# Performance work log

Measured on AMD Instinct MI355X. Metric: run time of the kernel, lower is better.

The kernel has to match this reference:

```python
import jax, jax.numpy as jnp
import numpy as np


def setup_inputs() -> dict:
    key = jax.random.key(0)
    k1, k2 = jax.random.split(key)
    B, N, D = 4, 2048, 1024
    context = jax.random.normal(k1, (B, N, D), dtype=jnp.float32)
    # Dense(embedding_dim*3): kernel [D, 3D], bias [3D] (glorot-ish scale)
    W_qkv = jax.random.normal(k2, (D, 3 * D), dtype=jnp.float32) * (1.0 / np.sqrt(D))
    b_qkv = jnp.zeros((3 * D,), dtype=jnp.float32)
    return {"context": context, "W_qkv": W_qkv, "b_qkv": b_qkv}


def reference(context, W_qkv, b_qkv):
    B, N, D = context.shape
    qkv = context @ W_qkv + b_qkv                       # [B, N, 3D]
    q, k, v = jnp.split(qkv, 3, axis=-1)                # each [B, N, D]
    scores = jnp.einsum("bnd,bmd->bnm", q, k)           # [B, N, N]
    # Faithful quirk: original divides by sqrt(scores.shape[-1]) == sqrt(N)
    scores = scores / jnp.asarray(np.sqrt(N), dtype=scores.dtype)
    causal = jnp.tril(jnp.ones((N, N), dtype=jnp.float32))  # lower-triangular
    scores = jnp.where(causal == 0, -jnp.inf, scores)
    probs = jax.nn.softmax(scores, axis=-1)             # [B, N, N]
    out = jnp.einsum("bnm,bmd->bnd", probs, v)          # [B, N, D]
    return out
```

## Files before the change

kernel.cpp:

```cpp
#include <hip/hip_runtime.h>
#include <cstdint>
#include <cstddef>


typedef __attribute__((ext_vector_type(8))) __bf16 bf16x8;
typedef __attribute__((ext_vector_type(4))) float f32x4;

__device__ inline unsigned short f2bf(float f) {
  unsigned u = __float_as_uint(f);
  u = (u + 0x7FFFu + ((u >> 16) & 1u)) >> 16;
  return (unsigned short)u;
}

__device__ inline void gld16(const void* g, void* l) {
  __builtin_amdgcn_global_load_lds(
      (const __attribute__((address_space(1))) unsigned int*)g,
      (__attribute__((address_space(3))) unsigned int*)l, 16, 0, 0);
}

__device__ inline void mma_mainloop(const unsigned short* Abase, long strideA,
                                    const unsigned short* Bbase, long strideB,
                                    int kIters, f32x4 acc[4][4]) {
  __shared__ unsigned short As[128 * 64];
  __shared__ unsigned short Bs[128 * 64];
  const int tid = threadIdx.x;
  const int lane = tid & 63;
  const int wave = tid >> 6;
  const int ry = (wave >> 1) * 64;
  const int rx = (wave & 1) * 64;
  const int lrow = lane >> 3;
  const int lchunk = (lane & 7) ^ lrow;
  const int lcol = lchunk * 8;

#pragma unroll
  for (int mi = 0; mi < 4; mi++)
#pragma unroll
    for (int nj = 0; nj < 4; nj++) acc[mi][nj] = (f32x4)(0.f);

  for (int kt = 0; kt < kIters; kt++) {
    const int k0 = kt * 64;
    __syncthreads();
#pragma unroll
    for (int c = 0; c < 4; c++) {
      const int q = wave * 4 + c;
      const int row = q * 8 + lrow;
      gld16(Abase + (size_t)row * strideA + k0 + lcol, &As[q * 512]);
      gld16(Bbase + (size_t)row * strideB + k0 + lcol, &Bs[q * 512]);
    }
    __syncthreads();
#pragma unroll
    for (int kk = 0; kk < 64; kk += 32) {
      const int cbase = (kk >> 3) + (lane >> 4);
      const int csw = ((cbase ^ (lane & 7)) << 3);
      bf16x8 a[4], b[4];
#pragma unroll
      for (int mi = 0; mi < 4; mi++)
        a[mi] = *(const bf16x8*)&As[(ry + mi * 16 + (lane & 15)) * 64 + csw];
#pragma unroll
      for (int nj = 0; nj < 4; nj++)
        b[nj] = *(const bf16x8*)&Bs[(rx + nj * 16 + (lane & 15)) * 64 + csw];
#pragma unroll
      for (int mi = 0; mi < 4; mi++)
#pragma unroll
        for (int nj = 0; nj < 4; nj++)
          acc[mi][nj] = __builtin_amdgcn_mfma_f32_16x16x32_bf16(a[mi], b[nj], acc[mi][nj], 0, 0, 0);
    }
  }
}


__global__ void k_convert(const float* __restrict__ x, unsigned short* __restrict__ y, int n4) {
  int i = blockIdx.x * blockDim.x + threadIdx.x;
  if (i >= n4) return;
  float4 v = ((const float4*)x)[i];
  ushort4 o;
  o.x = f2bf(v.x); o.y = f2bf(v.y); o.z = f2bf(v.z); o.w = f2bf(v.w);
  ((ushort4*)y)[i] = o;
}

__global__ void k_transpose_w(const float* __restrict__ W, unsigned short* __restrict__ Wt) {
  __shared__ unsigned short sm[64 * 65];
  const int n0 = blockIdx.x * 64;
  const int k0 = blockIdx.y * 64;
  for (int i = threadIdx.x; i < 4096; i += 256) {
    int r = i >> 6, c = i & 63;
    sm[c * 65 + r] = f2bf(W[(size_t)(k0 + r) * 3072 + n0 + c]);
  }
  __syncthreads();
  for (int i = threadIdx.x; i < 4096; i += 256) {
    int r = i >> 6, c = i & 63;
    Wt[(size_t)(n0 + r) * 1024 + k0 + c] = sm[r * 65 + c];
  }
}

__global__ void k_transpose_v(const unsigned short* __restrict__ qkv, unsigned short* __restrict__ vT) {
  __shared__ unsigned short sm[64 * 65];
  const int b = blockIdx.z;
  const int d0 = blockIdx.x * 64;
  const int n0 = blockIdx.y * 64;
  const unsigned short* src = qkv + ((size_t)b * 2048) * 3072 + 2048;
  for (int i = threadIdx.x; i < 4096; i += 256) {
    int r = i >> 6, c = i & 63;
    sm[c * 65 + r] = src[(size_t)(n0 + r) * 3072 + d0 + c];
  }
  __syncthreads();
  unsigned short* dst = vT + ((size_t)b * 1024) * 2048;
  for (int i = threadIdx.x; i < 4096; i += 256) {
    int r = i >> 6, c = i & 63;
    dst[(size_t)(d0 + r) * 2048 + n0 + c] = sm[r * 65 + c];
  }
}


__global__ __launch_bounds__(256) void k_gemm_qkv(const unsigned short* __restrict__ A,
                                                  const unsigned short* __restrict__ Bt,
                                                  const float* __restrict__ bias,
                                                  unsigned short* __restrict__ C) {
  f32x4 acc[4][4];
  const int tN0 = blockIdx.x * 128;
  const int tM0 = blockIdx.y * 128;
  mma_mainloop(A + (size_t)tM0 * 1024, 1024, Bt + (size_t)tN0 * 1024, 1024, 16, acc);
  const int lane = threadIdx.x & 63, wave = threadIdx.x >> 6;
  const int ry = (wave >> 1) * 64, rx = (wave & 1) * 64;
  const int col0 = lane & 15, rq = lane >> 4;
#pragma unroll
  for (int mi = 0; mi < 4; mi++)
#pragma unroll
    for (int nj = 0; nj < 4; nj++) {
      const int n = tN0 + rx + nj * 16 + col0;
      const float bv = bias[n];
#pragma unroll
      for (int r = 0; r < 4; r++) {
        const int m = tM0 + ry + mi * 16 + rq * 4 + r;
        C[(size_t)m * 3072 + n] = f2bf(acc[mi][nj][r] + bv);
      }
    }
}

__global__ __launch_bounds__(256) void k_scores(const unsigned short* __restrict__ qkv,
                                                unsigned short* __restrict__ P,
                                                float* __restrict__ l, float scale) {
  const int t = blockIdx.x, b = blockIdx.z;
  int qb = (int)((sqrtf(8.0f * (float)t + 1.0f) - 1.0f) * 0.5f);
  while (qb * (qb + 1) / 2 > t) qb--;
  while ((qb + 1) * (qb + 2) / 2 <= t) qb++;
  const int kb = t - qb * (qb + 1) / 2;
  f32x4 acc[4][4];
  const unsigned short* A = qkv + ((size_t)(b * 2048 + qb * 128)) * 3072;
  const unsigned short* B = qkv + ((size_t)(b * 2048 + kb * 128)) * 3072 + 1024;
  mma_mainloop(A, 3072, B, 3072, 16, acc);
  const int lane = threadIdx.x & 63, wave = threadIdx.x >> 6;
  const int ry = (wave >> 1) * 64, rx = (wave & 1) * 64;
  const int col0 = lane & 15, rq = lane >> 4;
  unsigned short* Pb = P + ((size_t)(b * 2048 + qb * 128)) * 2048 + (size_t)kb * 128;
  float* lb = l + b * 2048 + qb * 128;
#pragma unroll
  for (int mi = 0; mi < 4; mi++) {
#pragma unroll
    for (int r = 0; r < 4; r++) {
      const int m_local = ry + mi * 16 + rq * 4 + r;
      const int qi = qb * 128 + m_local;
      float rowpart = 0.f;
#pragma unroll
      for (int nj = 0; nj < 4; nj++) {
        const int n_local = rx + nj * 16 + col0;
        const int kj = kb * 128 + n_local;
        float p = 0.f;
        if (kj <= qi) p = __expf(acc[mi][nj][r] * scale);
        rowpart += p;
        Pb[(size_t)m_local * 2048 + n_local] = f2bf(p);
      }
      for (int off = 1; off < 16; off <<= 1) rowpart += __shfl_xor(rowpart, off, 64);
      if (col0 == 0) atomicAdd(&lb[m_local], rowpart);
    }
  }
}

__global__ __launch_bounds__(256) void k_pv(const unsigned short* __restrict__ P,
                                            const unsigned short* __restrict__ vT,
                                            const float* __restrict__ l,
                                            float* __restrict__ out) {
  const int db = blockIdx.x, qb = blockIdx.y, b = blockIdx.z;
  f32x4 acc[4][4];
  const unsigned short* A = P + ((size_t)(b * 2048 + qb * 128)) * 2048;
  const unsigned short* B = vT + ((size_t)(b * 1024 + db * 128)) * 2048;
  mma_mainloop(A, 2048, B, 2048, (qb + 1) * 2, acc);
  const int lane = threadIdx.x & 63, wave = threadIdx.x >> 6;
  const int ry = (wave >> 1) * 64, rx = (wave & 1) * 64;
  const int col0 = lane & 15, rq = lane >> 4;
  const float* lb = l + b * 2048 + qb * 128;
  float* ob = out + ((size_t)(b * 2048 + qb * 128)) * 1024 + db * 128;
#pragma unroll
  for (int mi = 0; mi < 4; mi++)
#pragma unroll
    for (int r = 0; r < 4; r++) {
      const int m_local = ry + mi * 16 + rq * 4 + r;
      const float inv = 1.0f / lb[m_local];
#pragma unroll
      for (int nj = 0; nj < 4; nj++) {
        const int n_local = rx + nj * 16 + col0;
        ob[(size_t)m_local * 1024 + n_local] = acc[mi][nj][r] * inv;
      }
    }
}


extern "C" void kernel_launch(void* const* d_in, const int* in_sizes, int n_in,
                              void* d_out, int out_size, void* d_ws, size_t ws_size,
                              hipStream_t stream) {
  const float* ctx  = (const float*)d_in[0];
  const float* W    = (const float*)d_in[1];
  const float* bias = (const float*)d_in[2];
  float* out = (float*)d_out;

  char* ws = (char*)d_ws;
  unsigned short* Actx = (unsigned short*)(ws + 0);
  unsigned short* Wt   = (unsigned short*)(ws + 16777216);
  unsigned short* qkv  = (unsigned short*)(ws + 23068672);
  unsigned short* vT   = (unsigned short*)(ws + 73400320);
  unsigned short* P    = (unsigned short*)(ws + 90177536);
  float*          lsum = (float*)(ws + 123731968);

  hipMemsetAsync(lsum, 0, 4 * 2048 * sizeof(float), stream);
  k_convert<<<8192, 256, 0, stream>>>(ctx, Actx, (8192 * 1024) / 4);
  k_transpose_w<<<dim3(48, 16), 256, 0, stream>>>(W, Wt);
  k_gemm_qkv<<<dim3(24, 64), 256, 0, stream>>>(Actx, Wt, bias, qkv);
  k_transpose_v<<<dim3(16, 32, 4), 256, 0, stream>>>(qkv, vT);
  k_scores<<<dim3(136, 1, 4), 256, 0, stream>>>(qkv, P, lsum, 0.022097086912079608f);
  k_pv<<<dim3(8, 16, 4), 256, 0, stream>>>(P, vT, lsum, out);
}
```

Measured before the change: 262.3 us.

## Fuse V transpose into QKV GEMM epilogue and vectorize epilogue stores

The QKV projection now writes Q and K to a packed buffer and writes V already transposed through its epilogue, which removes the separate V-transpose kernel and its extra global traffic. A templated MFMA operand swap makes each lane's four accumulators contiguous along the output column. Epilogues in all three GEMMs can then use 4-wide vector stores, and the row-sum shuffle reduction shrinks. The PV kernel also reverses the query-block order for half the batches to balance the causal workload across the grid.

New measurement: 257.0 us. 1.02x faster.

```diff
diff --git a/kernel.cpp b/kernel.cpp
--- a/kernel.cpp
+++ b/kernel.cpp
@@ -18,19 +18,18 @@
       (__attribute__((address_space(3))) unsigned int*)l, 16, 0, 0);
 }
 
-__device__ inline void mma_mainloop(const unsigned short* Abase, long strideA,
+template <bool SWAP>
+__device__ inline void mma_mainloop(unsigned short* As, unsigned short* Bs,
+                                    const unsigned short* Abase, long strideA,
                                     const unsigned short* Bbase, long strideB,
                                     int kIters, f32x4 acc[4][4]) {
-  __shared__ unsigned short As[128 * 64];
-  __shared__ unsigned short Bs[128 * 64];
   const int tid = threadIdx.x;
   const int lane = tid & 63;
   const int wave = tid >> 6;
   const int ry = (wave >> 1) * 64;
   const int rx = (wave & 1) * 64;
   const int lrow = lane >> 3;
-  const int lchunk = (lane & 7) ^ lrow;
-  const int lcol = lchunk * 8;
+  const int lcol = ((lane & 7) ^ lrow) * 8;
 
 #pragma unroll
   for (int mi = 0; mi < 4; mi++)
@@ -63,7 +62,9 @@
       for (int mi = 0; mi < 4; mi++)
 #pragma unroll
         for (int nj = 0; nj < 4; nj++)
-          acc[mi][nj] = __builtin_amdgcn_mfma_f32_16x16x32_bf16(a[mi], b[nj], acc[mi][nj], 0, 0, 0);
+          acc[mi][nj] = SWAP
+            ? __builtin_amdgcn_mfma_f32_16x16x32_bf16(b[nj], a[mi], acc[mi][nj], 0, 0, 0)
+            : __builtin_amdgcn_mfma_f32_16x16x32_bf16(a[mi], b[nj], acc[mi][nj], 0, 0, 0);
     }
   }
 }
@@ -93,86 +94,103 @@
   }
 }
 
-__global__ void k_transpose_v(const unsigned short* __restrict__ qkv, unsigned short* __restrict__ vT) {
-  __shared__ unsigned short sm[64 * 65];
-  const int b = blockIdx.z;
-  const int d0 = blockIdx.x * 64;
-  const int n0 = blockIdx.y * 64;
-  const unsigned short* src = qkv + ((size_t)b * 2048) * 3072 + 2048;
-  for (int i = threadIdx.x; i < 4096; i += 256) {
-    int r = i >> 6, c = i & 63;
-    sm[c * 65 + r] = src[(size_t)(n0 + r) * 3072 + d0 + c];
-  }
-  __syncthreads();
-  unsigned short* dst = vT + ((size_t)b * 1024) * 2048;
-  for (int i = threadIdx.x; i < 4096; i += 256) {
-    int r = i >> 6, c = i & 63;
-    dst[(size_t)(d0 + r) * 2048 + n0 + c] = sm[r * 65 + c];
-  }
-}
-
 
 __global__ __launch_bounds__(256) void k_gemm_qkv(const unsigned short* __restrict__ A,
-                                                  const unsigned short* __restrict__ Bt,
+                                                  const unsigned short* __restrict__ Wt,
                                                   const float* __restrict__ bias,
-                                                  unsigned short* __restrict__ C) {
+                                                  unsigned short* __restrict__ qk,
+                                                  unsigned short* __restrict__ vT) {
+  __shared__ unsigned short As[128 * 64];
+  __shared__ unsigned short Bs[128 * 64];
   f32x4 acc[4][4];
-  const int tN0 = blockIdx.x * 128;
   const int tM0 = blockIdx.y * 128;
-  mma_mainloop(A + (size_t)tM0 * 1024, 1024, Bt + (size_t)tN0 * 1024, 1024, 16, acc);
   const int lane = threadIdx.x & 63, wave = threadIdx.x >> 6;
   const int ry = (wave >> 1) * 64, rx = (wave & 1) * 64;
-  const int col0 = lane & 15, rq = lane >> 4;
-#pragma unroll
-  for (int mi = 0; mi < 4; mi++)
+  const int l16 = lane & 15, rq = lane >> 4;
+
+  if (blockIdx.x < 16) {
+    const int tN0 = blockIdx.x * 128;
+    mma_mainloop<true>(As, Bs, A + (size_t)tM0 * 1024, 1024,
+                       Wt + (size_t)tN0 * 1024, 1024, 16, acc);
+#pragma unroll
+    for (int mi = 0; mi < 4; mi++) {
+      const int m = tM0 + ry + mi * 16 + l16;
+#pragma unroll
+      for (int nj = 0; nj < 4; nj++) {
+        const int n = tN0 + rx + nj * 16 + rq * 4;
+        const float4 bv = *(const float4*)&bias[n];
+        ushort4 o;
+        o.x = f2bf(acc[mi][nj][0] + bv.x);
+        o.y = f2bf(acc[mi][nj][1] + bv.y);
+        o.z = f2bf(acc[mi][nj][2] + bv.z);
+        o.w = f2bf(acc[mi][nj][3] + bv.w);
+        *(ushort4*)&qk[(size_t)m * 2048 + n] = o;
+      }
+    }
+  } else {
+    const int tN0 = (blockIdx.x - 16) * 128;
+    mma_mainloop<false>(As, Bs, A + (size_t)tM0 * 1024, 1024,
+                        Wt + (size_t)(2048 + tN0) * 1024, 1024, 16, acc);
 #pragma unroll
     for (int nj = 0; nj < 4; nj++) {
-      const int n = tN0 + rx + nj * 16 + col0;
-      const float bv = bias[n];
-#pragma unroll
-      for (int r = 0; r < 4; r++) {
-        const int m = tM0 + ry + mi * 16 + rq * 4 + r;
-        C[(size_t)m * 3072 + n] = f2bf(acc[mi][nj][r] + bv);
+      const int d = tN0 + rx + nj * 16 + l16;
+      const float bv = bias[2048 + d];
+#pragma unroll
+      for (int mi = 0; mi < 4; mi++) {
+        const int m = tM0 + ry + mi * 16 + rq * 4;
+        const int b = m >> 11, ns = m & 2047;
+        ushort4 o;
+        o.x = f2bf(acc[mi][nj][0] + bv);
+        o.y = f2bf(acc[mi][nj][1] + bv);
+        o.z = f2bf(acc[mi][nj][2] + bv);
+        o.w = f2bf(acc[mi][nj][3] + bv);
+        *(ushort4*)&vT[((size_t)(b * 1024 + d)) * 2048 + ns] = o;
       }
     }
-}
-
-__global__ __launch_bounds__(256) void k_scores(const unsigned short* __restrict__ qkv,
+  }
+}
+
+__global__ __launch_bounds__(256) void k_scores(const unsigned short* __restrict__ qk,
                                                 unsigned short* __restrict__ P,
                                                 float* __restrict__ l, float scale) {
+  __shared__ unsigned short As[128 * 64];
+  __shared__ unsigned short Bs[128 * 64];
   const int t = blockIdx.x, b = blockIdx.z;
   int qb = (int)((sqrtf(8.0f * (float)t + 1.0f) - 1.0f) * 0.5f);
   while (qb * (qb + 1) / 2 > t) qb--;
   while ((qb + 1) * (qb + 2) / 2 <= t) qb++;
   const int kb = t - qb * (qb + 1) / 2;
   f32x4 acc[4][4];
-  const unsigned short* A = qkv + ((size_t)(b * 2048 + qb * 128)) * 3072;
-  const unsigned short* B = qkv + ((size_t)(b * 2048 + kb * 128)) * 3072 + 1024;
-  mma_mainloop(A, 3072, B, 3072, 16, acc);
+  const unsigned short* Aq = qk + ((size_t)(b * 2048 + qb * 128)) * 2048;
+  const unsigned short* Bk = qk + ((size_t)(b * 2048 + kb * 128)) * 2048 + 1024;
+  mma_mainloop<true>(As, Bs, Aq, 2048, Bk, 2048, 16, acc);
   const int lane = threadIdx.x & 63, wave = threadIdx.x >> 6;
   const int ry = (wave >> 1) * 64, rx = (wave & 1) * 64;
-  const int col0 = lane & 15, rq = lane >> 4;
+  const int l16 = lane & 15, rq = lane >> 4;
   unsigned short* Pb = P + ((size_t)(b * 2048 + qb * 128)) * 2048 + (size_t)kb * 128;
   float* lb = l + b * 2048 + qb * 128;
 #pragma unroll
   for (int mi = 0; mi < 4; mi++) {
-#pragma unroll
-    for (int r = 0; r < 4; r++) {
-      const int m_local = ry + mi * 16 + rq * 4 + r;
-      const int qi = qb * 128 + m_local;
-      float rowpart = 0.f;
-#pragma unroll
-      for (int nj = 0; nj < 4; nj++) {
-        const int n_local = rx + nj * 16 + col0;
-        const int kj = kb * 128 + n_local;
-        float p = 0.f;
-        if (kj <= qi) p = __expf(acc[mi][nj][r] * scale);
+    const int m_local = ry + mi * 16 + l16;
+    const int qi = qb * 128 + m_local;
+    float rowpart = 0.f;
+#pragma unroll
+    for (int nj = 0; nj < 4; nj++) {
+      const int n_base = rx + nj * 16 + rq * 4;
+      ushort4 o;
+      float p;
+#pragma unroll
+      for (int r = 0; r < 4; r++) {
+        const int kj = kb * 128 + n_base + r;
+        p = (kj <= qi) ? __expf(acc[mi][nj][r] * scale) : 0.f;
         rowpart += p;
-        Pb[(size_t)m_local * 2048 + n_local] = f2bf(p);
+        ((unsigned short*)&o)[r] = f2bf(p);
       }
-      for (int off = 1; off < 16; off <<= 1) rowpart += __shfl_xor(rowpart, off, 64);
-      if (col0 == 0) atomicAdd(&lb[m_local], rowpart);
-    }
+      *(ushort4*)&Pb[(size_t)m_local * 2048 + n_base] = o;
+    }
+    rowpart += __shfl_xor(rowpart, 16, 64);
+    rowpart += __shfl_xor(rowpart, 32, 64);
+    if (rq == 0) atomicAdd(&lb[m_local], rowpart);
   }
 }
 
@@ -180,28 +198,35 @@
                                             const unsigned short* __restrict__ vT,
                                             const float* __restrict__ l,
                                             float* __restrict__ out) {
-  const int db = blockIdx.x, qb = blockIdx.y, b = blockIdx.z;
+  __shared__ unsigned short As[128 * 64];
+  __shared__ unsigned short Bs[128 * 64];
+  const int db = blockIdx.x, b = blockIdx.z;
+  int qb = blockIdx.y;
+  if (b & 2) qb = 15 - qb;
   f32x4 acc[4][4];
-  const unsigned short* A = P + ((size_t)(b * 2048 + qb * 128)) * 2048;
-  const unsigned short* B = vT + ((size_t)(b * 1024 + db * 128)) * 2048;
-  mma_mainloop(A, 2048, B, 2048, (qb + 1) * 2, acc);
+  const unsigned short* Ap = P + ((size_t)(b * 2048 + qb * 128)) * 2048;
+  const unsigned short* Bv = vT + ((size_t)(b * 1024 + db * 128)) * 2048;
+  mma_mainloop<true>(As, Bs, Ap, 2048, Bv, 2048, (qb + 1) * 2, acc);
   const int lane = threadIdx.x & 63, wave = threadIdx.x >> 6;
   const int ry = (wave >> 1) * 64, rx = (wave & 1) * 64;
-  const int col0 = lane & 15, rq = lane >> 4;
+  const int l16 = lane & 15, rq = lane >> 4;
   const float* lb = l + b * 2048 + qb * 128;
   float* ob = out + ((size_t)(b * 2048 + qb * 128)) * 1024 + db * 128;
 #pragma unroll
-  for (int mi = 0; mi < 4; mi++)
-#pragma unroll
-    for (int r = 0; r < 4; r++) {
-      const int m_local = ry + mi * 16 + rq * 4 + r;
-      const float inv = 1.0f / lb[m_local];
-#pragma unroll
-      for (int nj = 0; nj < 4; nj++) {
-        const int n_local = rx + nj * 16 + col0;
-        ob[(size_t)m_local * 1024 + n_local] = acc[mi][nj][r] * inv;
-      }
-    }
+  for (int mi = 0; mi < 4; mi++) {
+    const int m_local = ry + mi * 16 + l16;
+    const float inv = 1.0f / lb[m_local];
+#pragma unroll
+    for (int nj = 0; nj < 4; nj++) {
+      const int n_base = rx + nj * 16 + rq * 4;
+      float4 o;
+      o.x = acc[mi][nj][0] * inv;
+      o.y = acc[mi][nj][1] * inv;
+      o.z = acc[mi][nj][2] * inv;
+      o.w = acc[mi][nj][3] * inv;
+      *(float4*)&ob[(size_t)m_local * 1024 + n_base] = o;
+    }
+  }
 }
 
 
@@ -216,16 +241,15 @@
   char* ws = (char*)d_ws;
   unsigned short* Actx = (unsigned short*)(ws + 0);
   unsigned short* Wt   = (unsigned short*)(ws + 16777216);
-  unsigned short* qkv  = (unsigned short*)(ws + 23068672);
-  unsigned short* vT   = (unsigned short*)(ws + 73400320);
-  unsigned short* P    = (unsigned short*)(ws + 90177536);
-  float*          lsum = (float*)(ws + 123731968);
+  unsigned short* qk   = (unsigned short*)(ws + 23068672);
+  unsigned short* vT   = (unsigned short*)(ws + 56623104);
+  unsigned short* P    = (unsigned short*)(ws + 73400320);
+  float*          lsum = (float*)(ws + 106954752);
 
   hipMemsetAsync(lsum, 0, 4 * 2048 * sizeof(float), stream);
   k_convert<<<8192, 256, 0, stream>>>(ctx, Actx, (8192 * 1024) / 4);
   k_transpose_w<<<dim3(48, 16), 256, 0, stream>>>(W, Wt);
-  k_gemm_qkv<<<dim3(24, 64), 256, 0, stream>>>(Actx, Wt, bias, qkv);
-  k_transpose_v<<<dim3(16, 32, 4), 256, 0, stream>>>(qkv, vT);
-  k_scores<<<dim3(136, 1, 4), 256, 0, stream>>>(qkv, P, lsum, 0.022097086912079608f);
+  k_gemm_qkv<<<dim3(24, 64), 256, 0, stream>>>(Actx, Wt, bias, qk, vT);
+  k_scores<<<dim3(136, 1, 4), 256, 0, stream>>>(qk, P, lsum, 0.022097086912079608f);
   k_pv<<<dim3(8, 16, 4), 256, 0, stream>>>(P, vT, lsum, out);
 }
```
